# Kernel optimization log

Hardware: AMD Instinct MI355X
Metric: run time of the kernel (lower is better)

## Reference

```python
import jax, jax.numpy as jnp
import numpy as np

# Standard SMPL 24-joint kinematic tree (parent of joint i); parent[0] is the root.
PARENTS = np.array([0, 0, 0, 0, 1, 2, 3, 4, 5, 6, 7, 8, 9, 9, 9, 12,
                    13, 14, 16, 17, 18, 19, 20, 21], dtype=np.int64)

B, J, V = 256, 24, 6890


def setup_inputs() -> dict:
    key = jax.random.key(0)
    k1, k2, k3, k4 = jax.random.split(key, 4)
    rot_mats = jax.random.normal(k1, (B, J, 3, 3), dtype=jnp.float32)
    joints = jax.random.normal(k2, (B, J, 3), dtype=jnp.float32)
    vertices = jax.random.normal(k3, (B, V, 3), dtype=jnp.float32)
    w = jax.random.uniform(k4, (V, J), dtype=jnp.float32)
    lbs_weights = w / jnp.sum(w, axis=-1, keepdims=True)  # convex skinning weights
    return {"rot_mats": rot_mats, "joints": joints,
            "vertices": vertices, "lbs_weights": lbs_weights}


def _transform_mat(R, t):
    """R: (...,3,3), t: (...,3) -> homogeneous (...,4,4), same as torch transform_mat."""
    top = jnp.concatenate([R, t[..., None]], axis=-1)  # (...,3,4)
    bottom = jnp.broadcast_to(jnp.array([0.0, 0.0, 0.0, 1.0], dtype=R.dtype),
                              top.shape[:-2] + (1, 4))
    return jnp.concatenate([top, bottom], axis=-2)


def reference(rot_mats, joints, vertices, lbs_weights):
    # --- batch_rigid_transform ---
    # relative joint offsets w.r.t. parent
    rel_joints = joints.at[:, 1:].add(-joints[:, PARENTS[1:]])  # (B,J,3)
    T_local = _transform_mat(rot_mats, rel_joints)              # (B,J,4,4)

    # forward kinematics chain: static unroll over the fixed 24-joint tree
    chain = [T_local[:, 0]]
    for i in range(1, J):
        chain.append(chain[int(PARENTS[i])] @ T_local[:, i])
    A = jnp.stack(chain, axis=1)                                # (B,J,4,4) world transforms

    posed_joints = A[:, :, :3, 3]                               # (B,J,3)

    # rel_transforms = A - pad(A @ [j;0]) : subtract transformed rest joint from last column
    tj = jnp.einsum('bjmn,bjn->bjm', A[:, :, :, :3], joints)    # (B,J,4)
    rel_transforms = A.at[:, :, :, 3].add(-tj)                  # (B,J,4,4)

    # --- linear blend skinning ---
    T = jnp.einsum('vj,bjmn->bvmn', lbs_weights, rel_transforms)  # (B,V,4,4)
    ones = jnp.ones(vertices.shape[:-1] + (1,), dtype=vertices.dtype)
    v_h = jnp.concatenate([vertices, ones], axis=-1)              # (B,V,4)
    posed_verts = jnp.einsum('bvmn,bvn->bvm', T, v_h)[..., :3]    # (B,V,3)

    return posed_verts, posed_joints, rel_transforms
```

## Files before the change

kernel.cpp:

```cpp
#include <hip/hip_runtime.h>

#define NB 256
#define NJ 24
#define NV 6890
#define VPB 256

__device__ __constant__ int ANC[4][NJ] = {
  {-1, 0, 0, 0, 1, 2, 3, 4, 5, 6, 7, 8, 9, 9, 9,12,13,14,16,17,18,19,20,21},
  {-1,-1,-1,-1, 0, 0, 0, 1, 2, 3, 4, 5, 6, 6, 6, 9, 9, 9,13,14,16,17,18,19},
  {-1,-1,-1,-1,-1,-1,-1,-1,-1,-1, 0, 0, 0, 0, 0, 3, 3, 3, 6, 6, 9, 9,13,14},
  {-1,-1,-1,-1,-1,-1,-1,-1,-1,-1,-1,-1,-1,-1,-1,-1,-1,-1,-1,-1,-1,-1, 0, 0}};

__global__ __launch_bounds__(288) void chain2(
    const float* __restrict__ rot,
    const float* __restrict__ joints,
    float* __restrict__ posed_joints,
    float* __restrict__ rel_tf)
{
    __shared__ float Jl[NJ * 3];
    __shared__ float MA[NJ * 12];
    __shared__ float MB[NJ * 12];
    const int b = blockIdx.x, tid = threadIdx.x;
    const int j = tid / 12, e = tid % 12, r = e >> 2, c = e & 3;
    constexpr int par[NJ] = {0,0,0,0,1,2,3,4,5,6,7,8,9,9,9,12,13,14,16,17,18,19,20,21};

    if (tid < NJ * 3) Jl[tid] = joints[(size_t)b * NJ * 3 + tid];
    __syncthreads();

    float tv;
    if (c < 3) {
        tv = rot[(size_t)b * NJ * 9 + j * 9 + r * 3 + c];
    } else {
        tv = Jl[j * 3 + r];
        if (j > 0) tv -= Jl[par[j] * 3 + r];
    }
    MA[j * 12 + e] = tv;
    __syncthreads();

#define DSTEP(SRC, DST, K)                                                 \
    do {                                                                   \
        const int a = ANC[K][j];                                           \
        float nv;                                                          \
        if (a < 0) {                                                       \
            nv = SRC[j * 12 + e];                                          \
        } else {                                                           \
            nv = SRC[a * 12 + r * 4 + 0] * SRC[j * 12 + 0 + c]            \
               + SRC[a * 12 + r * 4 + 1] * SRC[j * 12 + 4 + c]            \
               + SRC[a * 12 + r * 4 + 2] * SRC[j * 12 + 8 + c];           \
            if (c == 3) nv += SRC[a * 12 + r * 4 + 3];                    \
        }                                                                  \
        DST[j * 12 + e] = nv;                                              \
        __syncthreads();                                                   \
    } while (0)

    DSTEP(MA, MB, 0);
    DSTEP(MB, MA, 1);
    DSTEP(MA, MB, 2);
    DSTEP(MB, MA, 3);

    const float aje = MA[j * 12 + e];
    if (c == 3) {
        posed_joints[(size_t)b * NJ * 3 + j * 3 + r] = aje;
        const float tj = MA[j * 12 + r * 4 + 0] * Jl[j * 3 + 0]
                       + MA[j * 12 + r * 4 + 1] * Jl[j * 3 + 1]
                       + MA[j * 12 + r * 4 + 2] * Jl[j * 3 + 2];
        rel_tf[(size_t)b * NJ * 16 + j * 16 + e] = aje - tj;
    } else {
        rel_tf[(size_t)b * NJ * 16 + j * 16 + e] = aje;
    }
    if (tid < NJ * 4) {
        const int j2 = tid >> 2, c2 = tid & 3;
        rel_tf[(size_t)b * NJ * 16 + j2 * 16 + 12 + c2] = (c2 == 3) ? 1.0f : 0.0f;
    }
}

__global__ __launch_bounds__(VPB) void lbs3(
    const float* __restrict__ verts,
    const float* __restrict__ wgt,
    const float* __restrict__ rel_tf,
    float* __restrict__ out_verts)
{
    __shared__ float Wlds[VPB * 25];
    __shared__ float Mlds[NJ * 16];
    __shared__ float Vio[VPB * 3];
    const int tid = threadIdx.x;
    const int b = blockIdx.y;
    const int v0 = blockIdx.x * VPB;
    const int nvalid = min(VPB, NV - v0);

    for (int i = tid; i < NJ * 16; i += VPB)
        Mlds[i] = rel_tf[(size_t)b * NJ * 16 + i];

    {
        const float4* wg = reinterpret_cast<const float4*>(wgt + (size_t)v0 * NJ);
        const int nf4 = nvalid * NJ / 4;
        for (int i = tid; i < nf4; i += VPB) {
            const float4 q = wg[i];
            const int f = i * 4;
            const int v = f / NJ, j = f % NJ;
            float* d = &Wlds[v * 25 + j];
            d[0] = q.x; d[1] = q.y; d[2] = q.z; d[3] = q.w;
        }
    }

    {
        const float2* vg = reinterpret_cast<const float2*>(verts + ((size_t)b * NV + v0) * 3);
        const int nf2 = nvalid * 3 / 2;
        for (int i = tid; i < nf2; i += VPB) {
            const float2 q = vg[i];
            Vio[i * 2 + 0] = q.x;
            Vio[i * 2 + 1] = q.y;
        }
    }
    __syncthreads();

    float o0 = 0.0f, o1 = 0.0f, o2 = 0.0f;
    if (tid < nvalid) {
        const float x = Vio[tid * 3 + 0];
        const float y = Vio[tid * 3 + 1];
        const float z = Vio[tid * 3 + 2];

        float w[NJ];
#pragma unroll
        for (int j = 0; j < NJ; ++j) w[j] = Wlds[tid * 25 + j];

        float acc[12];
#pragma unroll
        for (int q = 0; q < 12; ++q) acc[q] = 0.0f;

        const float4* M4 = reinterpret_cast<const float4*>(Mlds);
#pragma unroll 4
        for (int j = 0; j < NJ; ++j) {
            const float4 m0 = M4[j * 4 + 0];
            const float4 m1 = M4[j * 4 + 1];
            const float4 m2 = M4[j * 4 + 2];
            const float wj = w[j];
            acc[0] += wj * m0.x; acc[1]  += wj * m0.y; acc[2]  += wj * m0.z; acc[3]  += wj * m0.w;
            acc[4] += wj * m1.x; acc[5]  += wj * m1.y; acc[6]  += wj * m1.z; acc[7]  += wj * m1.w;
            acc[8] += wj * m2.x; acc[9]  += wj * m2.y; acc[10] += wj * m2.z; acc[11] += wj * m2.w;
        }

        o0 = acc[0] * x + acc[1] * y + acc[2]  * z + acc[3];
        o1 = acc[4] * x + acc[5] * y + acc[6]  * z + acc[7];
        o2 = acc[8] * x + acc[9] * y + acc[10] * z + acc[11];
    }
    __syncthreads();
    if (tid < nvalid) {
        Vio[tid * 3 + 0] = o0;
        Vio[tid * 3 + 1] = o1;
        Vio[tid * 3 + 2] = o2;
    }
    __syncthreads();

    {
        float2* og = reinterpret_cast<float2*>(out_verts + ((size_t)b * NV + v0) * 3);
        const int nf2 = nvalid * 3 / 2;
        for (int i = tid; i < nf2; i += VPB)
            og[i] = make_float2(Vio[i * 2 + 0], Vio[i * 2 + 1]);
    }
}

extern "C" void kernel_launch(void* const* d_in, const int* in_sizes, int n_in,
                              void* d_out, int out_size, void* d_ws, size_t ws_size,
                              hipStream_t stream) {
    const float* rot     = (const float*)d_in[0];
    const float* joints  = (const float*)d_in[1];
    const float* verts   = (const float*)d_in[2];
    const float* weights = (const float*)d_in[3];

    float* out = (float*)d_out;
    float* posed_verts  = out;
    float* posed_joints = out + (size_t)NB * NV * 3;
    float* rel_tf       = posed_joints + (size_t)NB * NJ * 3;

    chain2<<<NB, 288, 0, stream>>>(rot, joints, posed_joints, rel_tf);

    const int nbx = (NV + VPB - 1) / VPB;
    lbs3<<<dim3(nbx, NB), VPB, 0, stream>>>(verts, weights, rel_tf, posed_verts);
}
```

Before: 112.0 us.

## Transpose skinning weights to joint-major and process four vertices per thread

A new pre-pass kernel transposes the vertex-major skinning weights into a joint-major, padded buffer in workspace. The skinning kernel then reads weights directly from global memory with coalesced float4 loads instead of staging them in shared memory. Each thread now handles four vertices per block of 1024, which raises register reuse of the joint matrices. The cost is an extra kernel launch, more registers per thread, and reads of uninitialized padding past the last valid vertex, whose results are discarded.

```diff
diff --git a/kernel.cpp b/kernel.cpp
--- a/kernel.cpp
+++ b/kernel.cpp
@@ -3,7 +3,29 @@
 #define NB 256
 #define NJ 24
 #define NV 6890
-#define VPB 256
+#define WT_LD 7168
+
+__global__ __launch_bounds__(256) void transpose_w2(const float* __restrict__ w,
+                                                    float* __restrict__ wT) {
+    __shared__ float Wl[256 * 25];
+    const int v0 = blockIdx.x * 256, tid = threadIdx.x;
+    const int nvalid = min(256, NV - v0);
+
+    const float4* wg = reinterpret_cast<const float4*>(w + (size_t)v0 * NJ);
+    const int nf4 = nvalid * NJ / 4;
+    for (int i = tid; i < nf4; i += 256) {
+        const float4 q = wg[i];
+        const int f = i * 4, v = f / NJ, j = f % NJ;
+        float* d = &Wl[v * 25 + j];
+        d[0] = q.x; d[1] = q.y; d[2] = q.z; d[3] = q.w;
+    }
+    __syncthreads();
+
+#pragma unroll
+    for (int j = 0; j < NJ; ++j)
+        for (int v = tid; v < nvalid; v += 256)
+            wT[(size_t)j * WT_LD + v0 + v] = Wl[v * 25 + j];
+}
 
 __device__ __constant__ int ANC[4][NJ] = {
   {-1, 0, 0, 0, 1, 2, 3, 4, 5, 6, 7, 8, 9, 9, 9,12,13,14,16,17,18,19,20,21},
@@ -74,89 +96,100 @@
     }
 }
 
-__global__ __launch_bounds__(VPB) void lbs3(
+#define LVPB 1024
+#define LTH 256
+
+__global__ __launch_bounds__(LTH) void lbs4(
     const float* __restrict__ verts,
-    const float* __restrict__ wgt,
+    const float* __restrict__ wT,
     const float* __restrict__ rel_tf,
     float* __restrict__ out_verts)
 {
-    __shared__ float Wlds[VPB * 25];
-    __shared__ float Mlds[NJ * 16];
-    __shared__ float Vio[VPB * 3];
-    const int tid = threadIdx.x;
-    const int b = blockIdx.y;
-    const int v0 = blockIdx.x * VPB;
-    const int nvalid = min(VPB, NV - v0);
-
-    for (int i = tid; i < NJ * 16; i += VPB)
-        Mlds[i] = rel_tf[(size_t)b * NJ * 16 + i];
-
-    {
-        const float4* wg = reinterpret_cast<const float4*>(wgt + (size_t)v0 * NJ);
-        const int nf4 = nvalid * NJ / 4;
-        for (int i = tid; i < nf4; i += VPB) {
-            const float4 q = wg[i];
-            const int f = i * 4;
-            const int v = f / NJ, j = f % NJ;
-            float* d = &Wlds[v * 25 + j];
-            d[0] = q.x; d[1] = q.y; d[2] = q.z; d[3] = q.w;
-        }
-    }
+    __shared__ float Ml[NJ * 16];
+    __shared__ float Vio[LTH * 13];
+    const int b = blockIdx.y, tid = threadIdx.x;
+    const int v0 = blockIdx.x * LVPB;
+    const int nvalid = min(LVPB, NV - v0);
+
+    for (int i = tid; i < NJ * 16; i += LTH)
+        Ml[i] = rel_tf[(size_t)b * NJ * 16 + i];
 
     {
         const float2* vg = reinterpret_cast<const float2*>(verts + ((size_t)b * NV + v0) * 3);
         const int nf2 = nvalid * 3 / 2;
-        for (int i = tid; i < nf2; i += VPB) {
+        for (int i = tid; i < nf2; i += LTH) {
             const float2 q = vg[i];
-            Vio[i * 2 + 0] = q.x;
-            Vio[i * 2 + 1] = q.y;
-        }
-    }
-    __syncthreads();
-
-    float o0 = 0.0f, o1 = 0.0f, o2 = 0.0f;
-    if (tid < nvalid) {
-        const float x = Vio[tid * 3 + 0];
-        const float y = Vio[tid * 3 + 1];
-        const float z = Vio[tid * 3 + 2];
-
-        float w[NJ];
-#pragma unroll
-        for (int j = 0; j < NJ; ++j) w[j] = Wlds[tid * 25 + j];
-
-        float acc[12];
-#pragma unroll
-        for (int q = 0; q < 12; ++q) acc[q] = 0.0f;
-
-        const float4* M4 = reinterpret_cast<const float4*>(Mlds);
-#pragma unroll 4
-        for (int j = 0; j < NJ; ++j) {
-            const float4 m0 = M4[j * 4 + 0];
-            const float4 m1 = M4[j * 4 + 1];
-            const float4 m2 = M4[j * 4 + 2];
-            const float wj = w[j];
-            acc[0] += wj * m0.x; acc[1]  += wj * m0.y; acc[2]  += wj * m0.z; acc[3]  += wj * m0.w;
-            acc[4] += wj * m1.x; acc[5]  += wj * m1.y; acc[6]  += wj * m1.z; acc[7]  += wj * m1.w;
-            acc[8] += wj * m2.x; acc[9]  += wj * m2.y; acc[10] += wj * m2.z; acc[11] += wj * m2.w;
-        }
-
-        o0 = acc[0] * x + acc[1] * y + acc[2]  * z + acc[3];
-        o1 = acc[4] * x + acc[5] * y + acc[6]  * z + acc[7];
-        o2 = acc[8] * x + acc[9] * y + acc[10] * z + acc[11];
-    }
-    __syncthreads();
-    if (tid < nvalid) {
-        Vio[tid * 3 + 0] = o0;
-        Vio[tid * 3 + 1] = o1;
-        Vio[tid * 3 + 2] = o2;
-    }
+            const int f0 = 2 * i, f1 = 2 * i + 1;
+            Vio[(f0 / 12) * 13 + (f0 % 12)] = q.x;
+            Vio[(f1 / 12) * 13 + (f1 % 12)] = q.y;
+        }
+    }
+    __syncthreads();
+
+    float px[4], py[4], pz[4];
+#pragma unroll
+    for (int k = 0; k < 4; ++k) {
+        px[k] = Vio[tid * 13 + k * 3 + 0];
+        py[k] = Vio[tid * 13 + k * 3 + 1];
+        pz[k] = Vio[tid * 13 + k * 3 + 2];
+    }
+
+    float acc[4][12];
+#pragma unroll
+    for (int k = 0; k < 4; ++k)
+#pragma unroll
+        for (int q = 0; q < 12; ++q) acc[k][q] = 0.0f;
+
+    const int vbase = v0 + tid * 4;
+#pragma unroll
+    for (int jc = 0; jc < 3; ++jc) {
+        float4 wv[8];
+#pragma unroll
+        for (int l = 0; l < 8; ++l) {
+            const int j = jc * 8 + l;
+            wv[l] = *reinterpret_cast<const float4*>(wT + (size_t)j * WT_LD + vbase);
+        }
+#pragma unroll
+        for (int l = 0; l < 8; ++l) {
+            const int j = jc * 8 + l;
+            const float4 m0 = *reinterpret_cast<const float4*>(Ml + j * 16 + 0);
+            const float4 m1 = *reinterpret_cast<const float4*>(Ml + j * 16 + 4);
+            const float4 m2 = *reinterpret_cast<const float4*>(Ml + j * 16 + 8);
+            const float m[12] = {m0.x, m0.y, m0.z, m0.w, m1.x, m1.y,
+                                 m1.z, m1.w, m2.x, m2.y, m2.z, m2.w};
+            const float wk[4] = {wv[l].x, wv[l].y, wv[l].z, wv[l].w};
+#pragma unroll
+            for (int k = 0; k < 4; ++k)
+#pragma unroll
+                for (int q = 0; q < 12; ++q) acc[k][q] += wk[k] * m[q];
+        }
+    }
+
+    float o[4][3];
+#pragma unroll
+    for (int k = 0; k < 4; ++k)
+#pragma unroll
+        for (int r = 0; r < 3; ++r)
+            o[k][r] = acc[k][r * 4 + 0] * px[k] + acc[k][r * 4 + 1] * py[k] +
+                      acc[k][r * 4 + 2] * pz[k] + acc[k][r * 4 + 3];
+
+    __syncthreads();
+#pragma unroll
+    for (int k = 0; k < 4; ++k)
+        if (tid * 4 + k < nvalid) {
+#pragma unroll
+            for (int r = 0; r < 3; ++r) Vio[tid * 13 + k * 3 + r] = o[k][r];
+        }
     __syncthreads();
 
     {
         float2* og = reinterpret_cast<float2*>(out_verts + ((size_t)b * NV + v0) * 3);
         const int nf2 = nvalid * 3 / 2;
-        for (int i = tid; i < nf2; i += VPB)
-            og[i] = make_float2(Vio[i * 2 + 0], Vio[i * 2 + 1]);
+        for (int i = tid; i < nf2; i += LTH) {
+            const int f0 = 2 * i, f1 = 2 * i + 1;
+            og[i] = make_float2(Vio[(f0 / 12) * 13 + (f0 % 12)],
+                                Vio[(f1 / 12) * 13 + (f1 % 12)]);
+        }
     }
 }
 
@@ -172,9 +205,11 @@
     float* posed_verts  = out;
     float* posed_joints = out + (size_t)NB * NV * 3;
     float* rel_tf       = posed_joints + (size_t)NB * NJ * 3;
-
+    float* wT           = (float*)d_ws;
+
+    transpose_w2<<<(NV + 255) / 256, 256, 0, stream>>>(weights, wT);
     chain2<<<NB, 288, 0, stream>>>(rot, joints, posed_joints, rel_tf);
 
-    const int nbx = (NV + VPB - 1) / VPB;
-    lbs3<<<dim3(nbx, NB), VPB, 0, stream>>>(verts, weights, rel_tf, posed_verts);
-}
+    const int nbx = (NV + LVPB - 1) / LVPB;
+    lbs4<<<dim3(nbx, NB), LTH, 0, stream>>>(verts, wT, rel_tf, posed_verts);
+}
```

Result: slower. 140.1 us (+25.0%).

## Pre-transpose skinning weights to joint-major layout and read M directly from global

Applied to the files above, without the earlier changes.

A new kernel transposes the (V,J) skinning weights once per call into a joint-major workspace buffer with padded leading dimension. The LBS kernel then reads weights coalesced straight from global/L2 in chunks of four joints, dropping the per-block LDS staging of weights and transforms. This removes about 25 KB of LDS per block, which should raise occupancy and cut redundant weight staging across the 256 batch blocks. The cost is an extra kernel launch and a workspace write. Threads past nvalid now read workspace padding and uninitialised LDS, but their results are not stored.

```diff
diff --git a/kernel.cpp b/kernel.cpp
--- a/kernel.cpp
+++ b/kernel.cpp
@@ -3,7 +3,29 @@
 #define NB 256
 #define NJ 24
 #define NV 6890
-#define VPB 256
+#define WT_LD 7168
+
+__global__ __launch_bounds__(256) void transpose_w2(const float* __restrict__ w,
+                                                    float* __restrict__ wT) {
+    __shared__ float Wl[256 * 25];
+    const int v0 = blockIdx.x * 256, tid = threadIdx.x;
+    const int nvalid = min(256, NV - v0);
+
+    const float4* wg = reinterpret_cast<const float4*>(w + (size_t)v0 * NJ);
+    const int nf4 = nvalid * NJ / 4;
+    for (int i = tid; i < nf4; i += 256) {
+        const float4 q = wg[i];
+        const int f = i * 4, v = f / NJ, j = f % NJ;
+        float* d = &Wl[v * 25 + j];
+        d[0] = q.x; d[1] = q.y; d[2] = q.z; d[3] = q.w;
+    }
+    __syncthreads();
+
+#pragma unroll
+    for (int j = 0; j < NJ; ++j)
+        for (int v = tid; v < nvalid; v += 256)
+            wT[(size_t)j * WT_LD + v0 + v] = Wl[v * 25 + j];
+}
 
 __device__ __constant__ int ANC[4][NJ] = {
   {-1, 0, 0, 0, 1, 2, 3, 4, 5, 6, 7, 8, 9, 9, 9,12,13,14,16,17,18,19,20,21},
@@ -74,76 +96,61 @@
     }
 }
 
-__global__ __launch_bounds__(VPB) void lbs3(
+__global__ __launch_bounds__(256) void lbs6(
     const float* __restrict__ verts,
-    const float* __restrict__ wgt,
+    const float* __restrict__ wT,
     const float* __restrict__ rel_tf,
     float* __restrict__ out_verts)
 {
-    __shared__ float Wlds[VPB * 25];
-    __shared__ float Mlds[NJ * 16];
-    __shared__ float Vio[VPB * 3];
-    const int tid = threadIdx.x;
-    const int b = blockIdx.y;
-    const int v0 = blockIdx.x * VPB;
-    const int nvalid = min(VPB, NV - v0);
-
-    for (int i = tid; i < NJ * 16; i += VPB)
-        Mlds[i] = rel_tf[(size_t)b * NJ * 16 + i];
-
-    {
-        const float4* wg = reinterpret_cast<const float4*>(wgt + (size_t)v0 * NJ);
-        const int nf4 = nvalid * NJ / 4;
-        for (int i = tid; i < nf4; i += VPB) {
-            const float4 q = wg[i];
-            const int f = i * 4;
-            const int v = f / NJ, j = f % NJ;
-            float* d = &Wlds[v * 25 + j];
-            d[0] = q.x; d[1] = q.y; d[2] = q.z; d[3] = q.w;
-        }
-    }
+    __shared__ float Vio[256 * 3];
+    const int b = blockIdx.y, tid = threadIdx.x;
+    const int v0 = blockIdx.x * 256;
+    const int nvalid = min(256, NV - v0);
+    const float* __restrict__ Mb = rel_tf + (size_t)b * NJ * 16;
 
     {
         const float2* vg = reinterpret_cast<const float2*>(verts + ((size_t)b * NV + v0) * 3);
         const int nf2 = nvalid * 3 / 2;
-        for (int i = tid; i < nf2; i += VPB) {
+        for (int i = tid; i < nf2; i += 256) {
             const float2 q = vg[i];
-            Vio[i * 2 + 0] = q.x;
-            Vio[i * 2 + 1] = q.y;
+            Vio[2 * i + 0] = q.x;
+            Vio[2 * i + 1] = q.y;
         }
     }
     __syncthreads();
 
-    float o0 = 0.0f, o1 = 0.0f, o2 = 0.0f;
-    if (tid < nvalid) {
-        const float x = Vio[tid * 3 + 0];
-        const float y = Vio[tid * 3 + 1];
-        const float z = Vio[tid * 3 + 2];
+    const float x = Vio[tid * 3 + 0];
+    const float y = Vio[tid * 3 + 1];
+    const float z = Vio[tid * 3 + 2];
+    const int v = v0 + tid;
 
-        float w[NJ];
+    float acc[12];
 #pragma unroll
-        for (int j = 0; j < NJ; ++j) w[j] = Wlds[tid * 25 + j];
+    for (int q = 0; q < 12; ++q) acc[q] = 0.0f;
 
-        float acc[12];
+#pragma unroll 1
+    for (int jc = 0; jc < 6; ++jc) {
+        float w[4];
 #pragma unroll
-        for (int q = 0; q < 12; ++q) acc[q] = 0.0f;
+        for (int l = 0; l < 4; ++l)
+            w[l] = wT[(size_t)(jc * 4 + l) * WT_LD + v];
+#pragma unroll
+        for (int l = 0; l < 4; ++l) {
+            const int j = jc * 4 + l;
+            const float4 m0 = *reinterpret_cast<const float4*>(Mb + j * 16 + 0);
+            const float4 m1 = *reinterpret_cast<const float4*>(Mb + j * 16 + 4);
+            const float4 m2 = *reinterpret_cast<const float4*>(Mb + j * 16 + 8);
+            const float wl = w[l];
+            acc[0] += wl * m0.x; acc[1]  += wl * m0.y; acc[2]  += wl * m0.z; acc[3]  += wl * m0.w;
+            acc[4] += wl * m1.x; acc[5]  += wl * m1.y; acc[6]  += wl * m1.z; acc[7]  += wl * m1.w;
+            acc[8] += wl * m2.x; acc[9]  += wl * m2.y; acc[10] += wl * m2.z; acc[11] += wl * m2.w;
+        }
+    }
 
-        const float4* M4 = reinterpret_cast<const float4*>(Mlds);
-#pragma unroll 4
-        for (int j = 0; j < NJ; ++j) {
-            const float4 m0 = M4[j * 4 + 0];
-            const float4 m1 = M4[j * 4 + 1];
-            const float4 m2 = M4[j * 4 + 2];
-            const float wj = w[j];
-            acc[0] += wj * m0.x; acc[1]  += wj * m0.y; acc[2]  += wj * m0.z; acc[3]  += wj * m0.w;
-            acc[4] += wj * m1.x; acc[5]  += wj * m1.y; acc[6]  += wj * m1.z; acc[7]  += wj * m1.w;
-            acc[8] += wj * m2.x; acc[9]  += wj * m2.y; acc[10] += wj * m2.z; acc[11] += wj * m2.w;
-        }
+    const float o0 = acc[0] * x + acc[1] * y + acc[2]  * z + acc[3];
+    const float o1 = acc[4] * x + acc[5] * y + acc[6]  * z + acc[7];
+    const float o2 = acc[8] * x + acc[9] * y + acc[10] * z + acc[11];
 
-        o0 = acc[0] * x + acc[1] * y + acc[2]  * z + acc[3];
-        o1 = acc[4] * x + acc[5] * y + acc[6]  * z + acc[7];
-        o2 = acc[8] * x + acc[9] * y + acc[10] * z + acc[11];
-    }
     __syncthreads();
     if (tid < nvalid) {
         Vio[tid * 3 + 0] = o0;
@@ -155,8 +162,8 @@
     {
         float2* og = reinterpret_cast<float2*>(out_verts + ((size_t)b * NV + v0) * 3);
         const int nf2 = nvalid * 3 / 2;
-        for (int i = tid; i < nf2; i += VPB)
-            og[i] = make_float2(Vio[i * 2 + 0], Vio[i * 2 + 1]);
+        for (int i = tid; i < nf2; i += 256)
+            og[i] = make_float2(Vio[2 * i + 0], Vio[2 * i + 1]);
     }
 }
 
@@ -172,9 +179,11 @@
     float* posed_verts  = out;
     float* posed_joints = out + (size_t)NB * NV * 3;
     float* rel_tf       = posed_joints + (size_t)NB * NJ * 3;
+    float* wT           = (float*)d_ws;
 
+    transpose_w2<<<(NV + 255) / 256, 256, 0, stream>>>(weights, wT);
     chain2<<<NB, 288, 0, stream>>>(rot, joints, posed_joints, rel_tf);
 
-    const int nbx = (NV + VPB - 1) / VPB;
-    lbs3<<<dim3(nbx, NB), VPB, 0, stream>>>(verts, weights, rel_tf, posed_verts);
+    const int nbx = (NV + 255) / 256;
+    lbs6<<<dim3(nbx, NB), 256, 0, stream>>>(verts, wT, rel_tf, posed_verts);
 }
```

Result: faster. 102.6 us (-8.4%).
